# Performance work log

Hardware: AMD Instinct MI355X
Metric: run time of the kernel (lower is better)

The kernel has to match this reference:

```python
import jax, jax.numpy as jnp
import numpy as np

B, S, H = 32, 2048, 1024

def setup_inputs() -> dict:
    key = jax.random.key(0)
    ks = jax.random.split(key, 7)
    scale = 1.0 / np.sqrt(H)
    return {
        "hidden": jax.random.normal(ks[0], (B, H), jnp.float32),
        "encoder_outputs": jax.random.normal(ks[1], (B, S, H), jnp.float32),
        "W_h": jax.random.uniform(ks[2], (H, H), jnp.float32, -scale, scale),
        "b_h": jax.random.uniform(ks[3], (H,), jnp.float32, -scale, scale),
        "W_c": jax.random.uniform(ks[4], (H, H), jnp.float32, -scale, scale),
        "b_c": jax.random.uniform(ks[5], (H,), jnp.float32, -scale, scale),
        "v": jax.random.normal(ks[6], (H,), jnp.float32),
    }

def reference(hidden, encoder_outputs, W_h, b_h, W_c, b_c, v):
    # hidden: [B,H]; encoder_outputs: [B,S,H]
    hidden_proj = hidden @ W_h.T + b_h                      # [B,H]
    context_proj = jnp.einsum('bsh,oh->bso', encoder_outputs, W_c) + b_c  # [B,S,H]
    energy = jnp.tanh(hidden_proj[:, None, :] + context_proj)             # [B,S,H]
    scores = jnp.einsum('bsh,h->bs', energy, v)             # [B,S]
    attn = jax.nn.softmax(scores, axis=1)                   # [B,S]
    context = jnp.einsum('bs,bsh->bh', attn, encoder_outputs)  # [B,H]
    return (context, attn)
```

## Files before the change

kernel.cpp:

```cpp
#include <hip/hip_runtime.h>
#include <hip/hip_fp16.h>
#include <math.h>
#include <stdint.h>

#define B_ 32
#define S_ 2048
#define H_ 1024

typedef _Float16 f16;
typedef _Float16 f16x8 __attribute__((ext_vector_type(8)));
typedef _Float16 f16x4 __attribute__((ext_vector_type(4)));
typedef float    f32x4 __attribute__((ext_vector_type(4)));

__global__ void k_cvt_wc(const float* __restrict__ wc, f16* __restrict__ wc16) {
    int i = (blockIdx.x * 256 + threadIdx.x) * 4;
    float4 vv = *(const float4*)(wc + i);
    f16x4 h;
    h[0] = (f16)vv.x; h[1] = (f16)vv.y; h[2] = (f16)vv.z; h[3] = (f16)vv.w;
    *(f16x4*)(wc16 + i) = h;
}

__global__ void k_cvt_img(const float* __restrict__ src, f16* __restrict__ dst) {
    int bid = blockIdx.x;
    int rt = bid >> 4, kc = bid & 15;
    int tid = threadIdx.x;
    char* img = (char*)dst + ((size_t)bid << 15);
    #pragma unroll
    for (int i = 0; i < 8; ++i) {
        int gid = i * 256 + tid;
        int r = gid >> 3, kg = gid & 7;
        const float* s = src + ((size_t)(rt * 256 + r)) * H_ + kc * 64 + kg * 8;
        float4 lo = *(const float4*)s;
        float4 hi = *(const float4*)(s + 4);
        f16x8 h;
        h[0]=(f16)lo.x; h[1]=(f16)lo.y; h[2]=(f16)lo.z; h[3]=(f16)lo.w;
        h[4]=(f16)hi.x; h[5]=(f16)hi.y; h[6]=(f16)hi.z; h[7]=(f16)hi.w;
        int byte = r * 128 + ((kg * 16) ^ ((r & 7) << 4));
        *(f16x8*)(img + byte) = h;
    }
}

__global__ void k_hp(const float* __restrict__ hid, const float* __restrict__ Wh,
                     const float* __restrict__ bh, float* __restrict__ hp) {
    int wid  = (blockIdx.x * 256 + threadIdx.x) >> 6;
    int lane = threadIdx.x & 63;
    int b = wid >> 10, oo = wid & 1023;
    const float* hrow = hid + b * H_;
    const float* wrow = Wh + (size_t)oo * H_;
    float s = 0.f;
    #pragma unroll
    for (int i = 0; i < 16; ++i) {
        int k = i * 64 + lane;
        s += hrow[k] * wrow[k];
    }
    #pragma unroll
    for (int m = 32; m; m >>= 1) s += __shfl_xor(s, m);
    if (lane == 0) hp[wid] = s + bh[oo];
}

#define GLD(dst_, src_) __builtin_amdgcn_global_load_lds(                      \
    (const __attribute__((address_space(1))) uint32_t*)(src_),                 \
    (__attribute__((address_space(3))) uint32_t*)(dst_), 16, 0, 0)

#define STAGE_A(t_) do {                                                       \
    _Pragma("unroll")                                                          \
    for (int i_ = 0; i_ < 4; ++i_) {                                           \
        int off_ = (i_ * 512 + tid) * 16;                                      \
        GLD(&Als[(t_) & 1][off_], aimg + ((size_t)(t_) << 15) + off_);         \
    }                                                                          \
} while (0)

#define STAGE_B(t_) do {                                                       \
    _Pragma("unroll")                                                          \
    for (int i_ = 0; i_ < 4; ++i_) {                                           \
        int off_ = (i_ * 512 + tid) * 16;                                      \
        GLD(&Als[(t_) & 1][32768 + off_], bimg + ((size_t)(t_) << 15) + off_); \
    }                                                                          \
} while (0)

__global__ __launch_bounds__(512, 2) void k_gemm(
        const f16* __restrict__ enc16, const f16* __restrict__ wc16,
        const float* __restrict__ hp, const float* __restrict__ bc,
        const float* __restrict__ v, float* __restrict__ spart) {
    __shared__ __align__(16) char Als[2][65536];

    const int tid = threadIdx.x;
    const int hb  = blockIdx.x;
    const int o   = (hb & 7) * 128 + (hb >> 3);
    const int mtile = o >> 2, nt = o & 3;
    const int brow = mtile >> 3;
    const int lane = tid & 63, wid = tid >> 6;
    const int waveM = wid >> 2, waveN = wid & 3;
    const int g = lane >> 4, l15 = lane & 15;
    const int rsw = (l15 & 7) << 4;

    const char* aimg = (const char*)enc16 + ((size_t)mtile << 19);
    const char* bimg = (const char*)wc16  + ((size_t)nt    << 19);

    int abase[8];
    #pragma unroll
    for (int im = 0; im < 8; ++im)
        abase[im] = (waveM * 128 + im * 16 + l15) * 128;
    int bbase[4];
    #pragma unroll
    for (int in = 0; in < 4; ++in)
        bbase[in] = (waveN * 64 + in * 16 + l15) * 128;

    f32x4 acc[8][4];
    #pragma unroll
    for (int im = 0; im < 8; ++im)
        #pragma unroll
        for (int in = 0; in < 4; ++in) acc[im][in] = (f32x4){0.f, 0.f, 0.f, 0.f};

    STAGE_A(0);
    STAGE_B(0);

    #pragma unroll 1
    for (int kc = 0; kc < 16; ++kc) {
        __syncthreads();
        if (kc < 15) { STAGE_A(kc + 1); STAGE_B(kc + 1); }
        const char* buf = Als[kc & 1];
        #pragma unroll
        for (int ks = 0; ks < 2; ++ks) {
            const int coff = (ks * 64 + g * 16) ^ rsw;
            f16x8 bfv[4];
            #pragma unroll
            for (int in = 0; in < 4; ++in)
                bfv[in] = *(const f16x8*)(buf + 32768 + bbase[in] + coff);
            f16x8 af[8];
            #pragma unroll
            for (int im = 0; im < 8; ++im)
                af[im] = *(const f16x8*)(buf + abase[im] + coff);
            #pragma unroll
            for (int im = 0; im < 8; ++im)
                #pragma unroll
                for (int in = 0; in < 4; ++in)
                    acc[im][in] = __builtin_amdgcn_mfma_f32_16x16x32_f16(
                        af[im], bfv[in], acc[im][in], 0, 0, 0);
        }
    }

    float hpbcr[4], vr[4];
    #pragma unroll
    for (int in = 0; in < 4; ++in) {
        int col = nt * 256 + waveN * 64 + in * 16 + l15;
        hpbcr[in] = hp[brow * H_ + col] + bc[col];
        vr[in]    = v[col];
    }
    float* sc = (float*)Als;
    #pragma unroll
    for (int im = 0; im < 8; ++im) {
        #pragma unroll
        for (int r = 0; r < 4; ++r) {
            float s = 0.f;
            #pragma unroll
            for (int in = 0; in < 4; ++in) {
                float e = acc[im][in][r] + hpbcr[in];
                float ex = __expf(2.f * e);
                float th = 1.f - 2.f / (ex + 1.f);
                s = fmaf(th, vr[in], s);
            }
            s += __shfl_xor(s, 1); s += __shfl_xor(s, 2);
            s += __shfl_xor(s, 4); s += __shfl_xor(s, 8);
            if (l15 == 0) sc[wid * 128 + im * 16 + g * 4 + r] = s;
        }
    }
    __syncthreads();
    if (tid < 256) {
        int wm = tid >> 7, lr = tid & 127;
        float s = sc[(wm * 4 + 0) * 128 + lr] + sc[(wm * 4 + 1) * 128 + lr]
                + sc[(wm * 4 + 2) * 128 + lr] + sc[(wm * 4 + 3) * 128 + lr];
        spart[(size_t)nt * (B_ * S_) + (size_t)mtile * 256 + tid] = s;
    }
}
#undef STAGE_A
#undef STAGE_B
#undef GLD

__global__ __launch_bounds__(512, 2) void k_gemm_fb(
        const float* __restrict__ enc, const f16* __restrict__ wc16,
        const float* __restrict__ hp, const float* __restrict__ bc,
        const float* __restrict__ v, float* __restrict__ scores) {
    __shared__ f16 Als[2][64 * 128];
    const int tid = threadIdx.x;
    const int blk = blockIdx.x;
    const size_t m0 = (size_t)blk * 64;
    const int brow = blk >> 5;
    const int lane = tid & 63, wid = tid >> 6;
    const int g = lane >> 4, l15 = lane & 15;
    const int rsw = (l15 & 7) << 4;
    const int row0 = tid >> 4,         c80 = tid & 15;
    const int row1 = (512 + tid) >> 4, c81 = tid & 15;
    const int wb0 = row0 * 256 + ((c80 * 16) ^ ((row0 & 7) << 4));
    const int wb1 = row1 * 256 + ((c81 * 16) ^ ((row1 & 7) << 4));
    int boff[8];
    #pragma unroll
    for (int in = 0; in < 8; ++in)
        boff[in] = (wid * 128 + in * 16 + l15) * H_ + g * 8;
    int abase[4];
    #pragma unroll
    for (int im = 0; im < 4; ++im) abase[im] = (im * 16 + l15) * 256;
    f32x4 acc[4][8];
    #pragma unroll
    for (int im = 0; im < 4; ++im)
        #pragma unroll
        for (int in = 0; in < 8; ++in) acc[im][in] = (f32x4){0.f,0.f,0.f,0.f};
    float4 sr[2][2];
    {
        const float* s0 = enc + (m0 + row0) * H_ + c80 * 8;
        const float* s1 = enc + (m0 + row1) * H_ + c81 * 8;
        sr[0][0] = *(const float4*)s0; sr[0][1] = *(const float4*)(s0 + 4);
        sr[1][0] = *(const float4*)s1; sr[1][1] = *(const float4*)(s1 + 4);
    }
    for (int kc = 0; kc < 8; ++kc) {
        char* buf = (char*)Als[kc & 1];
        {
            f16x8 h0, h1;
            h0[0]=(f16)sr[0][0].x; h0[1]=(f16)sr[0][0].y; h0[2]=(f16)sr[0][0].z; h0[3]=(f16)sr[0][0].w;
            h0[4]=(f16)sr[0][1].x; h0[5]=(f16)sr[0][1].y; h0[6]=(f16)sr[0][1].z; h0[7]=(f16)sr[0][1].w;
            h1[0]=(f16)sr[1][0].x; h1[1]=(f16)sr[1][0].y; h1[2]=(f16)sr[1][0].z; h1[3]=(f16)sr[1][0].w;
            h1[4]=(f16)sr[1][1].x; h1[5]=(f16)sr[1][1].y; h1[6]=(f16)sr[1][1].z; h1[7]=(f16)sr[1][1].w;
            *(f16x8*)(buf + wb0) = h0;
            *(f16x8*)(buf + wb1) = h1;
        }
        __syncthreads();
        if (kc < 7) {
            const float* s0 = enc + (m0 + row0) * H_ + (kc + 1) * 128 + c80 * 8;
            const float* s1 = enc + (m0 + row1) * H_ + (kc + 1) * 128 + c81 * 8;
            sr[0][0] = *(const float4*)s0; sr[0][1] = *(const float4*)(s0 + 4);
            sr[1][0] = *(const float4*)s1; sr[1][1] = *(const float4*)(s1 + 4);
        }
        #pragma unroll
        for (int ks = 0; ks < 4; ++ks) {
            f16x8 bfv[8];
            #pragma unroll
            for (int in = 0; in < 8; ++in)
                bfv[in] = *(const f16x8*)(wc16 + boff[in] + kc * 128 + ks * 32);
            const int coff = (ks * 64 + g * 16) ^ rsw;
            f16x8 af[4];
            #pragma unroll
            for (int im = 0; im < 4; ++im)
                af[im] = *(const f16x8*)(buf + abase[im] + coff);
            #pragma unroll
            for (int im = 0; im < 4; ++im)
                #pragma unroll
                for (int in = 0; in < 8; ++in)
                    acc[im][in] = __builtin_amdgcn_mfma_f32_16x16x32_f16(
                        af[im], bfv[in], acc[im][in], 0, 0, 0);
        }
    }
    float hpbcr[8], vr[8];
    #pragma unroll
    for (int in = 0; in < 8; ++in) {
        int col = wid * 128 + in * 16 + l15;
        hpbcr[in] = hp[brow * H_ + col] + bc[col];
        vr[in]    = v[col];
    }
    float score[4][4];
    #pragma unroll
    for (int im = 0; im < 4; ++im)
        #pragma unroll
        for (int r = 0; r < 4; ++r) {
            float s = 0.f;
            #pragma unroll
            for (int in = 0; in < 8; ++in) {
                float e = acc[im][in][r] + hpbcr[in];
                float ex = __expf(2.f * e);
                float th = 1.f - 2.f / (ex + 1.f);
                s = fmaf(th, vr[in], s);
            }
            s += __shfl_xor(s, 1); s += __shfl_xor(s, 2);
            s += __shfl_xor(s, 4); s += __shfl_xor(s, 8);
            score[im][r] = s;
        }
    __syncthreads();
    float* sc = (float*)Als;
    if (l15 == 0) {
        #pragma unroll
        for (int im = 0; im < 4; ++im)
            #pragma unroll
            for (int r = 0; r < 4; ++r)
                sc[wid * 64 + im * 16 + g * 4 + r] = score[im][r];
    }
    __syncthreads();
    if (tid < 64) {
        float s = 0.f;
        #pragma unroll
        for (int w = 0; w < 8; ++w) s += sc[w * 64 + tid];
        scores[m0 + tid] = s;
    }
}

__global__ void k_softmax4(const float* __restrict__ spart, float* __restrict__ attn) {
    __shared__ float red[4], red2[4];
    int b = blockIdx.x, tid = threadIdx.x, lane = tid & 63, w = tid >> 6;
    const float* sp = spart + (size_t)b * S_;
    float lv[8];
    float mx = -1e30f;
    #pragma unroll
    for (int i = 0; i < 8; ++i) {
        size_t r = (size_t)i * 256 + tid;
        lv[i] = sp[r] + sp[(size_t)(B_*S_) + r]
              + sp[2*(size_t)(B_*S_) + r] + sp[3*(size_t)(B_*S_) + r];
        mx = fmaxf(mx, lv[i]);
    }
    #pragma unroll
    for (int m = 32; m; m >>= 1) mx = fmaxf(mx, __shfl_xor(mx, m));
    if (lane == 0) red[w] = mx;
    __syncthreads();
    mx = fmaxf(fmaxf(red[0], red[1]), fmaxf(red[2], red[3]));
    float sum = 0.f;
    #pragma unroll
    for (int i = 0; i < 8; ++i) { lv[i] = expf(lv[i] - mx); sum += lv[i]; }
    #pragma unroll
    for (int m = 32; m; m >>= 1) sum += __shfl_xor(sum, m);
    if (lane == 0) red2[w] = sum;
    __syncthreads();
    sum = red2[0] + red2[1] + red2[2] + red2[3];
    float inv = 1.f / sum;
    #pragma unroll
    for (int i = 0; i < 8; ++i) attn[b * S_ + i * 256 + tid] = lv[i] * inv;
}

__global__ void k_softmax(const float* __restrict__ scores, float* __restrict__ attn) {
    __shared__ float red[4], red2[4];
    int b = blockIdx.x, tid = threadIdx.x, lane = tid & 63, w = tid >> 6;
    const float* sc = scores + b * S_;
    float lv[8];
    float mx = -1e30f;
    #pragma unroll
    for (int i = 0; i < 8; ++i) { lv[i] = sc[i * 256 + tid]; mx = fmaxf(mx, lv[i]); }
    #pragma unroll
    for (int m = 32; m; m >>= 1) mx = fmaxf(mx, __shfl_xor(mx, m));
    if (lane == 0) red[w] = mx;
    __syncthreads();
    mx = fmaxf(fmaxf(red[0], red[1]), fmaxf(red[2], red[3]));
    float sum = 0.f;
    #pragma unroll
    for (int i = 0; i < 8; ++i) { lv[i] = expf(lv[i] - mx); sum += lv[i]; }
    #pragma unroll
    for (int m = 32; m; m >>= 1) sum += __shfl_xor(sum, m);
    if (lane == 0) red2[w] = sum;
    __syncthreads();
    sum = red2[0] + red2[1] + red2[2] + red2[3];
    float inv = 1.f / sum;
    #pragma unroll
    for (int i = 0; i < 8; ++i) attn[b * S_ + i * 256 + tid] = lv[i] * inv;
}

__global__ void k_ctxpart16(const f16* __restrict__ enc16, const float* __restrict__ attn,
                            float* __restrict__ cpart) {
    int bid = blockIdx.x, mtile = bid >> 4, kc = bid & 15;
    int b = mtile >> 3;
    int tid = threadIdx.x;
    int kg = tid & 7, q = tid >> 3;
    const char* img = (const char*)enc16 + ((size_t)bid << 15);
    const float* arow = attn + b * S_ + (mtile & 7) * 256;
    float acc[8] = {0,0,0,0,0,0,0,0};
    #pragma unroll 8
    for (int rr = 0; rr < 32; ++rr) {
        int r = q * 32 + rr;
        float a = arow[r];
        f16x8 e = *(const f16x8*)(img + r * 128 + ((kg * 16) ^ ((r & 7) << 4)));
        #pragma unroll
        for (int j = 0; j < 8; ++j) acc[j] = fmaf(a, (float)e[j], acc[j]);
    }
    float* dst = cpart + (size_t)(b * 64 + (mtile & 7) * 8 + q) * H_ + kc * 64 + kg * 8;
    #pragma unroll
    for (int j = 0; j < 8; ++j) dst[j] = acc[j];
}

__global__ void k_ctxpart(const float* __restrict__ enc, const float* __restrict__ attn,
                          float* __restrict__ cpart) {
    int b = blockIdx.x >> 5, chunk = blockIdx.x & 31;
    int t = threadIdx.x;
    const float* arow = attn + b * S_;
    f32x4 acc = {0.f, 0.f, 0.f, 0.f};
    for (int s0 = 0; s0 < 64; ++s0) {
        int s = chunk * 64 + s0;
        float a = arow[s];
        float4 e = *(const float4*)(enc + ((size_t)b * S_ + s) * H_ + t * 4);
        acc[0] += a * e.x; acc[1] += a * e.y; acc[2] += a * e.z; acc[3] += a * e.w;
    }
    *(f32x4*)(cpart + (size_t)blockIdx.x * H_ + t * 4) = acc;
}

__global__ void k_ctxreduce(const float* __restrict__ cpart, float* __restrict__ ctx, int nc) {
    int idx = blockIdx.x * 256 + threadIdx.x;
    int b = idx >> 10, h = idx & 1023;
    float s = 0.f;
    for (int c = 0; c < nc; ++c) s += cpart[((size_t)(b * nc + c)) * H_ + h];
    ctx[idx] = s;
}

extern "C" void kernel_launch(void* const* d_in, const int* in_sizes, int n_in,
                              void* d_out, int out_size, void* d_ws, size_t ws_size,
                              hipStream_t stream) {
    const float* hidden = (const float*)d_in[0];
    const float* enc    = (const float*)d_in[1];
    const float* Wh     = (const float*)d_in[2];
    const float* bh     = (const float*)d_in[3];
    const float* Wc     = (const float*)d_in[4];
    const float* bc     = (const float*)d_in[5];
    const float* v      = (const float*)d_in[6];
    float* out = (float*)d_out;
    (void)in_sizes; (void)n_in; (void)out_size;

    char* ws = (char*)d_ws;
    f16*   wc16   = (f16*)ws;
    float* hp     = (float*)(ws + (2u << 20));
    float* scores = (float*)(ws + (2u << 20) + (128u << 10));
    float* spart  = (float*)(ws + (2u << 20) + (384u << 10));
    float* cpart  = (float*)(ws + (4u << 20));
    f16*   enc16  = (f16*)(ws + (16u << 20));

    const size_t need_fast = (size_t)(16u << 20) + ((size_t)128 << 20);
    const bool fast = ws_size >= need_fast;

    float* attn = out + B_ * H_;

    hipLaunchKernelGGL(k_hp,      dim3(8192), dim3(256), 0, stream, hidden, Wh, bh, hp);
    if (fast) {
        hipLaunchKernelGGL(k_cvt_img,  dim3(64),   dim3(256), 0, stream, Wc, wc16);
        hipLaunchKernelGGL(k_cvt_img,  dim3(4096), dim3(256), 0, stream, enc, enc16);
        hipLaunchKernelGGL(k_gemm,     dim3(1024), dim3(512), 0, stream, enc16, wc16, hp, bc, v, spart);
        hipLaunchKernelGGL(k_softmax4, dim3(32),   dim3(256), 0, stream, spart, attn);
        hipLaunchKernelGGL(k_ctxpart16,dim3(4096), dim3(64),  0, stream, enc16, attn, cpart);
        hipLaunchKernelGGL(k_ctxreduce,dim3(128),  dim3(256), 0, stream, cpart, out, 64);
    } else {
        hipLaunchKernelGGL(k_cvt_wc,   dim3(1024), dim3(256), 0, stream, Wc, wc16);
        hipLaunchKernelGGL(k_gemm_fb,  dim3(1024), dim3(512), 0, stream, enc, wc16, hp, bc, v, scores);
        hipLaunchKernelGGL(k_softmax,  dim3(32),   dim3(256), 0, stream, scores, attn);
        hipLaunchKernelGGL(k_ctxpart,  dim3(1024), dim3(256), 0, stream, enc, attn, cpart);
        hipLaunchKernelGGL(k_ctxreduce,dim3(128),  dim3(256), 0, stream, cpart, out, 32);
    }
}
```

Measured before the change: 284.3 us.

## Split GEMM k-loop into fine-grained phases with interleaved staging and priority

Restructures the main GEMM loop into four phases per k-chunk, each issuing a portion of the next tile's global-to-LDS loads, waiting on partial vmcnt, and running MFMAs at raised priority between barriers. The goal is to overlap memory transfer with compute more finely than one bulk stage per chunk. It also rewrites the hidden projection kernel so each wave keeps two W_h rows in registers and loops over batch, which cuts W_h reloads and the launch to 128 blocks. The trade-offs are more barriers per iteration and a small-grid hp kernel that may leave the device underused.

```diff
diff --git a/kernel.cpp b/kernel.cpp
--- a/kernel.cpp
+++ b/kernel.cpp
@@ -42,40 +42,78 @@
 
 __global__ void k_hp(const float* __restrict__ hid, const float* __restrict__ Wh,
                      const float* __restrict__ bh, float* __restrict__ hp) {
-    int wid  = (blockIdx.x * 256 + threadIdx.x) >> 6;
-    int lane = threadIdx.x & 63;
-    int b = wid >> 10, oo = wid & 1023;
-    const float* hrow = hid + b * H_;
-    const float* wrow = Wh + (size_t)oo * H_;
-    float s = 0.f;
-    #pragma unroll
-    for (int i = 0; i < 16; ++i) {
-        int k = i * 64 + lane;
-        s += hrow[k] * wrow[k];
-    }
-    #pragma unroll
-    for (int m = 32; m; m >>= 1) s += __shfl_xor(s, m);
-    if (lane == 0) hp[wid] = s + bh[oo];
+    int tid = threadIdx.x, lane = tid & 63, w = tid >> 6;
+    int oo = blockIdx.x * 8 + w * 2;
+    const float* w0 = Wh + (size_t)oo * H_;
+    const float* w1 = Wh + (size_t)(oo + 1) * H_;
+    float wr0[16], wr1[16];
+    #pragma unroll
+    for (int i = 0; i < 16; ++i) { wr0[i] = w0[i*64+lane]; wr1[i] = w1[i*64+lane]; }
+    for (int b = 0; b < 32; ++b) {
+        const float* hrow = hid + b * H_;
+        float s0 = 0.f, s1 = 0.f;
+        #pragma unroll
+        for (int i = 0; i < 16; ++i) {
+            float h = hrow[i*64+lane];
+            s0 = fmaf(h, wr0[i], s0); s1 = fmaf(h, wr1[i], s1);
+        }
+        #pragma unroll
+        for (int m = 32; m; m >>= 1) { s0 += __shfl_xor(s0, m); s1 += __shfl_xor(s1, m); }
+        if (lane == 0) {
+            hp[b * H_ + oo]     = s0 + bh[oo];
+            hp[b * H_ + oo + 1] = s1 + bh[oo + 1];
+        }
+    }
 }
 
 #define GLD(dst_, src_) __builtin_amdgcn_global_load_lds(                      \
     (const __attribute__((address_space(1))) uint32_t*)(src_),                 \
     (__attribute__((address_space(3))) uint32_t*)(dst_), 16, 0, 0)
 
-#define STAGE_A(t_) do {                                                       \
+#define VMC(n_) asm volatile("s_waitcnt vmcnt(" #n_ ")" ::: "memory")
+#define BAR() asm volatile("s_barrier" ::: "memory")
+
+#define STG_A(t_, h_) do {                                                     \
+    _Pragma("unroll")                                                          \
+    for (int i_ = 0; i_ < 2; ++i_) {                                           \
+        int o_ = (h_) * 8192 + i_ * 16384 + tid * 16;                          \
+        GLD(&Als[(t_) & 1][o_], aimg + ((size_t)(t_) << 15) + o_);             \
+    }                                                                          \
+} while (0)
+#define STG_B(t_, rh_) do {                                                    \
+    _Pragma("unroll")                                                          \
+    for (int i_ = 0; i_ < 2; ++i_) {                                           \
+        int o_ = (rh_) * 16384 + i_ * 8192 + tid * 16;                         \
+        GLD(&Als[(t_) & 1][32768 + o_], bimg + ((size_t)(t_) << 15) + o_);     \
+    }                                                                          \
+} while (0)
+
+#define PH(kc_, ks_, h_, BB_, RB_, STG_, WT_) do {                             \
+    const char* buf_ = Als[(kc_) & 1];                                         \
+    const int coff_ = ((ks_) * 64 + g * 16) ^ rsw;                             \
+    if (RB_) {                                                                 \
+        _Pragma("unroll")                                                      \
+        for (int j_ = 0; j_ < 4; ++j_)                                         \
+            bfv[(BB_) + j_] = *(const f16x8*)(buf_ + 32768 + bbase[j_] + coff_); \
+    }                                                                          \
+    f16x8 af_[4];                                                              \
+    _Pragma("unroll")                                                          \
+    for (int i_ = 0; i_ < 4; ++i_)                                             \
+        af_[i_] = *(const f16x8*)(buf_ + abase[(h_) * 4 + i_] + coff_);        \
+    STG_;                                                                      \
+    WT_;                                                                       \
+    BAR();                                                                     \
+    __builtin_amdgcn_sched_barrier(0);                                         \
+    __builtin_amdgcn_s_setprio(1);                                             \
     _Pragma("unroll")                                                          \
     for (int i_ = 0; i_ < 4; ++i_) {                                           \
-        int off_ = (i_ * 512 + tid) * 16;                                      \
-        GLD(&Als[(t_) & 1][off_], aimg + ((size_t)(t_) << 15) + off_);         \
+        _Pragma("unroll")                                                      \
+        for (int j_ = 0; j_ < 4; ++j_)                                         \
+            acc[(h_) * 4 + i_][j_] = __builtin_amdgcn_mfma_f32_16x16x32_f16(   \
+                af_[i_], bfv[(BB_) + j_], acc[(h_) * 4 + i_][j_], 0, 0, 0);    \
     }                                                                          \
-} while (0)
-
-#define STAGE_B(t_) do {                                                       \
-    _Pragma("unroll")                                                          \
-    for (int i_ = 0; i_ < 4; ++i_) {                                           \
-        int off_ = (i_ * 512 + tid) * 16;                                      \
-        GLD(&Als[(t_) & 1][32768 + off_], bimg + ((size_t)(t_) << 15) + off_); \
-    }                                                                          \
+    __builtin_amdgcn_s_setprio(0);                                             \
+    BAR();                                                                     \
 } while (0)
 
 __global__ __launch_bounds__(512, 2) void k_gemm(
@@ -112,33 +150,23 @@
         #pragma unroll
         for (int in = 0; in < 4; ++in) acc[im][in] = (f32x4){0.f, 0.f, 0.f, 0.f};
 
-    STAGE_A(0);
-    STAGE_B(0);
+    f16x8 bfv[8];
+
+    STG_A(0, 0); STG_B(0, 0); STG_B(0, 1); STG_A(0, 1);
+    VMC(2);
+    BAR();
 
     #pragma unroll 1
-    for (int kc = 0; kc < 16; ++kc) {
-        __syncthreads();
-        if (kc < 15) { STAGE_A(kc + 1); STAGE_B(kc + 1); }
-        const char* buf = Als[kc & 1];
-        #pragma unroll
-        for (int ks = 0; ks < 2; ++ks) {
-            const int coff = (ks * 64 + g * 16) ^ rsw;
-            f16x8 bfv[4];
-            #pragma unroll
-            for (int in = 0; in < 4; ++in)
-                bfv[in] = *(const f16x8*)(buf + 32768 + bbase[in] + coff);
-            f16x8 af[8];
-            #pragma unroll
-            for (int im = 0; im < 8; ++im)
-                af[im] = *(const f16x8*)(buf + abase[im] + coff);
-            #pragma unroll
-            for (int im = 0; im < 8; ++im)
-                #pragma unroll
-                for (int in = 0; in < 4; ++in)
-                    acc[im][in] = __builtin_amdgcn_mfma_f32_16x16x32_f16(
-                        af[im], bfv[in], acc[im][in], 0, 0, 0);
-        }
-    }
+    for (int kc = 0; kc < 15; ++kc) {
+        PH(kc, 0, 0, 0, 1, STG_A(kc + 1, 0), ;);
+        PH(kc, 1, 0, 4, 1, STG_B(kc + 1, 0), VMC(4));
+        PH(kc, 0, 1, 0, 0, STG_B(kc + 1, 1), ;);
+        PH(kc, 1, 1, 4, 0, STG_A(kc + 1, 1), VMC(2));
+    }
+    PH(15, 0, 0, 0, 1, ;, ;);
+    PH(15, 1, 0, 4, 1, ;, VMC(0));
+    PH(15, 0, 1, 0, 0, ;, ;);
+    PH(15, 1, 1, 4, 0, ;, ;);
 
     float hpbcr[4], vr[4];
     #pragma unroll
@@ -173,8 +201,11 @@
         spart[(size_t)nt * (B_ * S_) + (size_t)mtile * 256 + tid] = s;
     }
 }
-#undef STAGE_A
-#undef STAGE_B
+#undef PH
+#undef STG_A
+#undef STG_B
+#undef VMC
+#undef BAR
 #undef GLD
 
 __global__ __launch_bounds__(512, 2) void k_gemm_fb(
@@ -419,7 +450,7 @@
 
     float* attn = out + B_ * H_;
 
-    hipLaunchKernelGGL(k_hp,      dim3(8192), dim3(256), 0, stream, hidden, Wh, bh, hp);
+    hipLaunchKernelGGL(k_hp,      dim3(128), dim3(256), 0, stream, hidden, Wh, bh, hp);
     if (fast) {
         hipLaunchKernelGGL(k_cvt_img,  dim3(64),   dim3(256), 0, stream, Wc, wc16);
         hipLaunchKernelGGL(k_cvt_img,  dim3(4096), dim3(256), 0, stream, enc, enc16);
```

New measurement: 309.4 us. +8.8%, slower.

## Fuse fp32-to-fp16 encoder conversion into GEMM A-tile loading

Applied to the files above, without the earlier changes.

Drops the separate k_cvt_img pass over encoder_outputs. The GEMM now loads fp32 encoder rows into registers, converts them to fp16, writes them into the swizzled LDS tile, and has one of the four N-tile blocks write the fp16 image out for the later context kernel. The main loop is unrolled by two with register double-buffering so global loads overlap the MFMA work. In exchange, every one of the four N-tile blocks sharing an M-tile now reads the fp32 A data (twice the bytes of fp16), and register pressure rises from the staging buffers.

```diff
diff --git a/kernel.cpp b/kernel.cpp
--- a/kernel.cpp
+++ b/kernel.cpp
@@ -62,14 +62,6 @@
     (const __attribute__((address_space(1))) uint32_t*)(src_),                 \
     (__attribute__((address_space(3))) uint32_t*)(dst_), 16, 0, 0)
 
-#define STAGE_A(t_) do {                                                       \
-    _Pragma("unroll")                                                          \
-    for (int i_ = 0; i_ < 4; ++i_) {                                           \
-        int off_ = (i_ * 512 + tid) * 16;                                      \
-        GLD(&Als[(t_) & 1][off_], aimg + ((size_t)(t_) << 15) + off_);         \
-    }                                                                          \
-} while (0)
-
 #define STAGE_B(t_) do {                                                       \
     _Pragma("unroll")                                                          \
     for (int i_ = 0; i_ < 4; ++i_) {                                           \
@@ -78,8 +70,55 @@
     }                                                                          \
 } while (0)
 
+#define LDA(t_, S_) do {                                                       \
+    _Pragma("unroll")                                                          \
+    for (int i_ = 0; i_ < 4; ++i_) {                                           \
+        const float* s_ = asrc + (size_t)(i_ * 64) * H_ + (t_) * 64;           \
+        S_[i_][0] = *(const float4*)s_;                                        \
+        S_[i_][1] = *(const float4*)(s_ + 4);                                  \
+    }                                                                          \
+} while (0)
+
+#define WRA(t_, S_) do {                                                       \
+    _Pragma("unroll")                                                          \
+    for (int i_ = 0; i_ < 4; ++i_) {                                           \
+        f16x8 h_;                                                              \
+        h_[0]=(f16)S_[i_][0].x; h_[1]=(f16)S_[i_][0].y;                        \
+        h_[2]=(f16)S_[i_][0].z; h_[3]=(f16)S_[i_][0].w;                        \
+        h_[4]=(f16)S_[i_][1].x; h_[5]=(f16)S_[i_][1].y;                        \
+        h_[6]=(f16)S_[i_][1].z; h_[7]=(f16)S_[i_][1].w;                        \
+        int off_ = (i_ * 512 + tid) * 16;                                      \
+        *(f16x8*)(&Als[(t_) & 1][off_]) = h_;                                  \
+        if (i_ == nt)                                                          \
+            *(f16x8*)(aimg16 + ((size_t)(t_) << 15) + off_) = h_;              \
+    }                                                                          \
+} while (0)
+
+#define COMP(kc_) do {                                                         \
+    const char* buf_ = Als[(kc_) & 1];                                         \
+    _Pragma("unroll")                                                          \
+    for (int ks_ = 0; ks_ < 2; ++ks_) {                                        \
+        const int coff_ = (ks_ * 64 + g * 16) ^ rsw;                           \
+        f16x8 bfv_[4];                                                         \
+        _Pragma("unroll")                                                      \
+        for (int in_ = 0; in_ < 4; ++in_)                                      \
+            bfv_[in_] = *(const f16x8*)(buf_ + 32768 + bbase[in_] + coff_);    \
+        f16x8 af_[8];                                                          \
+        _Pragma("unroll")                                                      \
+        for (int im_ = 0; im_ < 8; ++im_)                                      \
+            af_[im_] = *(const f16x8*)(buf_ + abase[im_] + coff_);             \
+        _Pragma("unroll")                                                      \
+        for (int im_ = 0; im_ < 8; ++im_)                                      \
+            _Pragma("unroll")                                                  \
+            for (int in_ = 0; in_ < 4; ++in_)                                  \
+                acc[im_][in_] = __builtin_amdgcn_mfma_f32_16x16x32_f16(        \
+                    af_[im_], bfv_[in_], acc[im_][in_], 0, 0, 0);              \
+    }                                                                          \
+} while (0)
+
 __global__ __launch_bounds__(512, 2) void k_gemm(
-        const f16* __restrict__ enc16, const f16* __restrict__ wc16,
+        const float* __restrict__ enc, const f16* __restrict__ wc16,
+        f16* __restrict__ enc16,
         const float* __restrict__ hp, const float* __restrict__ bc,
         const float* __restrict__ v, float* __restrict__ spart) {
     __shared__ __align__(16) char Als[2][65536];
@@ -94,8 +133,11 @@
     const int g = lane >> 4, l15 = lane & 15;
     const int rsw = (l15 & 7) << 4;
 
-    const char* aimg = (const char*)enc16 + ((size_t)mtile << 19);
-    const char* bimg = (const char*)wc16  + ((size_t)nt    << 19);
+    const int srow = tid >> 3;
+    const int skg  = (tid & 7) ^ (srow & 7);
+    const float* asrc = enc + ((size_t)mtile * 256 + srow) * H_ + skg * 8;
+    char* aimg16 = (char*)enc16 + ((size_t)mtile << 19);
+    const char* bimg = (const char*)wc16 + ((size_t)nt << 19);
 
     int abase[8];
     #pragma unroll
@@ -112,32 +154,24 @@
         #pragma unroll
         for (int in = 0; in < 4; ++in) acc[im][in] = (f32x4){0.f, 0.f, 0.f, 0.f};
 
-    STAGE_A(0);
+    float4 sA[4][2], sB[4][2];
+
+    LDA(0, sA);
     STAGE_B(0);
+    WRA(0, sA);
+    LDA(1, sB);
 
     #pragma unroll 1
-    for (int kc = 0; kc < 16; ++kc) {
+    for (int kc = 0; kc < 16; kc += 2) {
         __syncthreads();
-        if (kc < 15) { STAGE_A(kc + 1); STAGE_B(kc + 1); }
-        const char* buf = Als[kc & 1];
-        #pragma unroll
-        for (int ks = 0; ks < 2; ++ks) {
-            const int coff = (ks * 64 + g * 16) ^ rsw;
-            f16x8 bfv[4];
-            #pragma unroll
-            for (int in = 0; in < 4; ++in)
-                bfv[in] = *(const f16x8*)(buf + 32768 + bbase[in] + coff);
-            f16x8 af[8];
-            #pragma unroll
-            for (int im = 0; im < 8; ++im)
-                af[im] = *(const f16x8*)(buf + abase[im] + coff);
-            #pragma unroll
-            for (int im = 0; im < 8; ++im)
-                #pragma unroll
-                for (int in = 0; in < 4; ++in)
-                    acc[im][in] = __builtin_amdgcn_mfma_f32_16x16x32_f16(
-                        af[im], bfv[in], acc[im][in], 0, 0, 0);
-        }
+        WRA(kc + 1, sB);
+        STAGE_B(kc + 1);
+        if (kc < 14) LDA(kc + 2, sA);
+        COMP(kc);
+        __syncthreads();
+        if (kc + 1 < 15) { WRA(kc + 2, sA); STAGE_B(kc + 2); }
+        if (kc + 1 < 14) LDA(kc + 3, sB);
+        COMP(kc + 1);
     }
 
     float hpbcr[4], vr[4];
@@ -173,7 +207,9 @@
         spart[(size_t)nt * (B_ * S_) + (size_t)mtile * 256 + tid] = s;
     }
 }
-#undef STAGE_A
+#undef COMP
+#undef WRA
+#undef LDA
 #undef STAGE_B
 #undef GLD
 
@@ -422,8 +458,7 @@
     hipLaunchKernelGGL(k_hp,      dim3(8192), dim3(256), 0, stream, hidden, Wh, bh, hp);
     if (fast) {
         hipLaunchKernelGGL(k_cvt_img,  dim3(64),   dim3(256), 0, stream, Wc, wc16);
-        hipLaunchKernelGGL(k_cvt_img,  dim3(4096), dim3(256), 0, stream, enc, enc16);
-        hipLaunchKernelGGL(k_gemm,     dim3(1024), dim3(512), 0, stream, enc16, wc16, hp, bc, v, spart);
+        hipLaunchKernelGGL(k_gemm,     dim3(1024), dim3(512), 0, stream, enc, wc16, enc16, hp, bc, v, spart);
         hipLaunchKernelGGL(k_softmax4, dim3(32),   dim3(256), 0, stream, spart, attn);
         hipLaunchKernelGGL(k_ctxpart16,dim3(4096), dim3(64),  0, stream, enc16, attn, cpart);
         hipLaunchKernelGGL(k_ctxreduce,dim3(128),  dim3(256), 0, stream, cpart, out, 64);
```

Result: slower. 474.2 us (+66.8%).
